# Optimization experiments

Hardware: AMD Instinct MI355X
Metric: run time of the kernel (lower is better)

The kernel has to match this reference:

```python
import jax, jax.numpy as jnp
import numpy as np

N_NODES = 100000
N_EDGES = 400000
IN_F, HID, OUT_F = 128, 1024, 64


def gcn_conv(x, src, dst, ew, W, b, n):
    # PyG GCNConv: add self-loops (weight 1), symmetric normalization,
    # out[dst] += norm * (x @ W)[src], then bias.
    loop = jnp.arange(n)
    s = jnp.concatenate([src, loop])
    d = jnp.concatenate([dst, loop])
    w = jnp.concatenate([ew, jnp.ones((n,), dtype=ew.dtype)])
    deg = jax.ops.segment_sum(w, d, num_segments=n)
    dinv = jnp.where(deg > 0, jax.lax.rsqrt(deg), 0.0)
    norm = dinv[s] * w * dinv[d]                      # [E+N]
    h = x @ W                                         # [N, out]
    out = jax.ops.segment_sum(h[s] * norm[:, None], d, num_segments=n)
    return out + b


def setup_inputs() -> dict:
    key = jax.random.key(0)
    k = jax.random.split(key, 8)
    x = jax.random.normal(k[0], (N_NODES, IN_F), dtype=jnp.float32)
    edge_index = jax.random.randint(k[1], (2, N_EDGES), 0, N_NODES, dtype=jnp.int64)
    edge_weight = jax.random.uniform(k[2], (N_EDGES,), dtype=jnp.float32)
    # Glorot-ish init for params
    W1 = jax.random.normal(k[3], (IN_F, HID), dtype=jnp.float32) * (1.0 / np.sqrt(IN_F))
    b1 = jnp.zeros((HID,), dtype=jnp.float32)
    W2 = jax.random.normal(k[4], (HID, OUT_F), dtype=jnp.float32) * (1.0 / np.sqrt(HID))
    b2 = jnp.zeros((OUT_F,), dtype=jnp.float32)
    return {"x": x, "edge_index": edge_index, "edge_weight": edge_weight,
            "W1": W1, "b1": b1, "W2": W2, "b2": b2}


def reference(x, edge_index, edge_weight, W1, b1, W2, b2):
    src, dst = edge_index[0], edge_index[1]
    h = gcn_conv(x, src, dst, edge_weight, W1, b1, N_NODES)
    h = jax.nn.relu(h)
    # F.dropout with training=False is identity (eval mode)
    out = gcn_conv(h, src, dst, edge_weight, W2, b2, N_NODES)
    return out
```

## Files before the change

### kernel.cpp

```cpp
#include <hip/hip_runtime.h>
#include <hip/hip_bf16.h>

#define N_NODES 100000
#define N_EDGES 400000
#define IN_F    128
#define HID     1024
#define OUT_F   64
#define BUCKET_CAP 24

typedef __attribute__((ext_vector_type(8))) short short8;
typedef __attribute__((ext_vector_type(4))) float floatx4;

__device__ inline unsigned short f2bf(float f) {
    unsigned int u = __float_as_uint(f);
    unsigned int r = u + 0x7FFF + ((u >> 16) & 1);
    return (unsigned short)(r >> 16);
}

__device__ inline float bf2f(unsigned int lo16) {
    return __uint_as_float(lo16 << 16);
}

__device__ __forceinline__ void gload_lds16(const void* g, void* l) {
    __builtin_amdgcn_global_load_lds(
        (const __attribute__((address_space(1))) void*)g,
        (__attribute__((address_space(3))) void*)l, 16, 0, 0);
}


__global__ void init_kernel(float* __restrict__ deg, int* __restrict__ cnt, int n) {
    int i = blockIdx.x * blockDim.x + threadIdx.x;
    if (i < n) { deg[i] = 1.0f; cnt[i] = 0; }
}

__global__ void deg_accum_kernel(const int* __restrict__ dst, const float* __restrict__ w,
                                 float* __restrict__ deg, int E) {
    int e = blockIdx.x * blockDim.x + threadIdx.x;
    if (e < E) atomicAdd(&deg[dst[e]], w[e]);
}

__global__ void rsqrt_inplace_kernel(float* __restrict__ deg, int n) {
    int i = blockIdx.x * blockDim.x + threadIdx.x;
    if (i < n) deg[i] = rsqrtf(deg[i]);
}

__global__ void fill_pairs_kernel(const int* __restrict__ src, const int* __restrict__ dst,
                                  const float* __restrict__ w, const float* __restrict__ dinv,
                                  int* __restrict__ cnt, int2* __restrict__ pairs, int E) {
    int e = blockIdx.x * blockDim.x + threadIdx.x;
    if (e < E) {
        int s = src[e];
        int d = dst[e];
        float nv = dinv[s] * w[e] * dinv[d];
        int slot = atomicAdd(&cnt[d], 1);
        if (slot < BUCKET_CAP)
            pairs[(long)d * BUCKET_CAP + slot] = make_int2(s, __float_as_int(nv));
    }
}


__global__ void convert_xb_kernel(const float* __restrict__ in, unsigned short* __restrict__ out, long n8) {
    long i = (long)blockIdx.x * blockDim.x + threadIdx.x;
    if (i < n8) {
        float4 a = ((const float4*)in)[i * 2];
        float4 b = ((const float4*)in)[i * 2 + 1];
        unsigned int q0 = (unsigned int)f2bf(a.x) | ((unsigned int)f2bf(a.y) << 16);
        unsigned int q1 = (unsigned int)f2bf(a.z) | ((unsigned int)f2bf(a.w) << 16);
        unsigned int q2 = (unsigned int)f2bf(b.x) | ((unsigned int)f2bf(b.y) << 16);
        unsigned int q3 = (unsigned int)f2bf(b.z) | ((unsigned int)f2bf(b.w) << 16);
        ((uint4*)out)[i] = make_uint4(q0, q1, q2, q3);
    }
}


__global__ __launch_bounds__(256) void gather128_kernel(
    const int2* __restrict__ pairs, const int* __restrict__ cnt,
    const float* __restrict__ dinv, const unsigned short* __restrict__ xb,
    unsigned short* __restrict__ xab)
{
    int node = blockIdx.x * 4 + (threadIdx.x >> 6);
    int l = threadIdx.x & 63;
    float di = dinv[node];
    float s = di * di;
    unsigned int uv = ((const unsigned int*)(xb + (long)node * IN_F))[l];
    float2 acc;
    acc.x = bf2f(uv & 0xffffu) * s;
    acc.y = bf2f(uv >> 16) * s;
    int c = cnt[node]; c = c < BUCKET_CAP ? c : BUCKET_CAP;
    const int2* p = pairs + (long)node * BUCKET_CAP;
    int j = 0;
    for (; j + 4 <= c; j += 4) {
        int2 p0 = p[j], p1 = p[j + 1], p2 = p[j + 2], p3 = p[j + 3];
        unsigned int u0 = ((const unsigned int*)(xb + (long)p0.x * IN_F))[l];
        unsigned int u1 = ((const unsigned int*)(xb + (long)p1.x * IN_F))[l];
        unsigned int u2 = ((const unsigned int*)(xb + (long)p2.x * IN_F))[l];
        unsigned int u3 = ((const unsigned int*)(xb + (long)p3.x * IN_F))[l];
        float n0 = __int_as_float(p0.y), n1 = __int_as_float(p1.y);
        float n2 = __int_as_float(p2.y), n3 = __int_as_float(p3.y);
        acc.x += n0 * bf2f(u0 & 0xffffu) + n1 * bf2f(u1 & 0xffffu)
               + n2 * bf2f(u2 & 0xffffu) + n3 * bf2f(u3 & 0xffffu);
        acc.y += n0 * bf2f(u0 >> 16) + n1 * bf2f(u1 >> 16)
               + n2 * bf2f(u2 >> 16) + n3 * bf2f(u3 >> 16);
    }
    for (; j < c; j++) {
        int2 pp = p[j];
        float nv = __int_as_float(pp.y);
        unsigned int u = ((const unsigned int*)(xb + (long)pp.x * IN_F))[l];
        acc.x += nv * bf2f(u & 0xffffu);
        acc.y += nv * bf2f(u >> 16);
    }
    unsigned int pk = (unsigned int)f2bf(acc.x) | ((unsigned int)f2bf(acc.y) << 16);
    ((unsigned int*)(xab + (long)node * IN_F))[l] = pk;
}

__global__ __launch_bounds__(256) void gather64_kernel(
    const int2* __restrict__ pairs, const int* __restrict__ cnt,
    const float* __restrict__ dinv, const unsigned short* __restrict__ tb,
    const float* __restrict__ bias, float* __restrict__ out)
{
    int node = blockIdx.x * 8 + (threadIdx.x >> 5);
    int l = threadIdx.x & 31;
    float di = dinv[node];
    float s = di * di;
    unsigned int tv = ((const unsigned int*)(tb + (long)node * OUT_F))[l];
    float2 bb = ((const float2*)bias)[l];
    float2 acc;
    acc.x = bf2f(tv & 0xffffu) * s + bb.x;
    acc.y = bf2f(tv >> 16) * s + bb.y;
    int c = cnt[node]; c = c < BUCKET_CAP ? c : BUCKET_CAP;
    const int2* p = pairs + (long)node * BUCKET_CAP;
    int j = 0;
    for (; j + 4 <= c; j += 4) {
        int2 p0 = p[j], p1 = p[j + 1], p2 = p[j + 2], p3 = p[j + 3];
        unsigned int u0 = ((const unsigned int*)(tb + (long)p0.x * OUT_F))[l];
        unsigned int u1 = ((const unsigned int*)(tb + (long)p1.x * OUT_F))[l];
        unsigned int u2 = ((const unsigned int*)(tb + (long)p2.x * OUT_F))[l];
        unsigned int u3 = ((const unsigned int*)(tb + (long)p3.x * OUT_F))[l];
        float n0 = __int_as_float(p0.y), n1 = __int_as_float(p1.y);
        float n2 = __int_as_float(p2.y), n3 = __int_as_float(p3.y);
        acc.x += n0 * bf2f(u0 & 0xffffu) + n1 * bf2f(u1 & 0xffffu)
               + n2 * bf2f(u2 & 0xffffu) + n3 * bf2f(u3 & 0xffffu);
        acc.y += n0 * bf2f(u0 >> 16) + n1 * bf2f(u1 >> 16)
               + n2 * bf2f(u2 >> 16) + n3 * bf2f(u3 >> 16);
    }
    for (; j < c; j++) {
        int2 pp = p[j];
        float nv = __int_as_float(pp.y);
        unsigned int u = ((const unsigned int*)(tb + (long)pp.x * OUT_F))[l];
        acc.x += nv * bf2f(u & 0xffffu);
        acc.y += nv * bf2f(u >> 16);
    }
    ((float2*)(out + (long)node * OUT_F))[l] = acc;
}


__global__ void convert_wstream_kernel(const float* __restrict__ W1, const float* __restrict__ W2,
                                       unsigned short* __restrict__ S) {
    int r = blockIdx.x * blockDim.x + threadIdx.x;
    int c = blockIdx.y;
    int f = r >> 9;
    int l = (r >> 3) & 63;
    int j = r & 7;
    float v;
    if (f < 16) {
        int nt = f >> 2, kt = f & 3;
        int hid = c * 64 + nt * 16 + (l & 15);
        int k   = kt * 32 + (l >> 4) * 8 + j;
        v = W1[(long)k * HID + hid];
    } else {
        int f2 = f - 16;
        int kb = f2 >> 2, nt = f2 & 3;
        int kh = c * 64 + kb * 32 + (l >> 4) * 8 + j;
        int oc = nt * 16 + (l & 15);
        v = W2[(long)kh * OUT_F + oc];
    }
    S[(long)c * 12288 + r] = f2bf(v);
}


__global__ __launch_bounds__(512, 2) void fused_mlp_mfma_kernel(
    const unsigned short* __restrict__ Xb, const unsigned short* __restrict__ Wstream,
    const float* __restrict__ b1, unsigned short* __restrict__ Tb, int M)
{
    __shared__ unsigned short Wbuf[2][12288];
    __shared__ unsigned short Hs[8][4096];

    const int tid = threadIdx.x;
    const int w   = tid >> 6;
    const int l   = tid & 63;
    const int lr  = l & 15;
    const int lq  = l >> 4;
    const int swz = (lr & 7) << 4;
    const long row0 = (long)blockIdx.x * 512 + w * 64;

    short8 bx[4][4];
    #pragma unroll
    for (int rt = 0; rt < 4; rt++) {
        long row = row0 + rt * 16 + lr;
        if (row < M) {
            const unsigned short* p = Xb + row * IN_F + lq * 8;
            #pragma unroll
            for (int kt = 0; kt < 4; kt++)
                bx[rt][kt] = *(const short8*)(p + kt * 32);
        } else {
            #pragma unroll
            for (int kt = 0; kt < 4; kt++)
                #pragma unroll
                for (int j = 0; j < 8; j++) bx[rt][kt][j] = 0;
        }
    }

    {
        const unsigned short* g = Wstream + (long)(w * 3) * 512 + l * 8;
        unsigned short* d = &Wbuf[0][(w * 3) * 512];
        #pragma unroll
        for (int s = 0; s < 3; s++)
            gload_lds16(g + s * 512, d + s * 512);
    }
    __syncthreads();

    floatx4 tacc[4][4];
    #pragma unroll
    for (int rt = 0; rt < 4; rt++)
        #pragma unroll
        for (int nt = 0; nt < 4; nt++)
            tacc[rt][nt] = (floatx4)0.0f;

    for (int c = 0; c < 16; c++) {
        const int cur = c & 1;

        if (c < 15) {
            const unsigned short* g = Wstream + (long)(c + 1) * 12288 + (long)(w * 3) * 512 + l * 8;
            unsigned short* d = &Wbuf[cur ^ 1][(w * 3) * 512];
            #pragma unroll
            for (int s = 0; s < 3; s++)
                gload_lds16(g + s * 512, d + s * 512);
        }

        const unsigned short* Wb = &Wbuf[cur][0];
        char* slab = (char*)&Hs[w][0];

        #pragma unroll
        for (int nt = 0; nt < 4; nt++) {
            short8 w1f[4];
            #pragma unroll
            for (int kt = 0; kt < 4; kt++)
                w1f[kt] = *(const short8*)(Wb + (nt * 4 + kt) * 512 + l * 8);

            floatx4 hacc[4];
            #pragma unroll
            for (int rt = 0; rt < 4; rt++) hacc[rt] = (floatx4)0.0f;

            #pragma unroll
            for (int kt = 0; kt < 4; kt++)
                #pragma unroll
                for (int rt = 0; rt < 4; rt++)
                    hacc[rt] = __builtin_amdgcn_mfma_f32_16x16x32_bf16(w1f[kt], bx[rt][kt], hacc[rt], 0, 0, 0);

            floatx4 bb = *(const floatx4*)(b1 + c * 64 + nt * 16 + lq * 4);
            #pragma unroll
            for (int rt = 0; rt < 4; rt++) {
                float h0 = fmaxf(hacc[rt][0] + bb[0], 0.0f);
                float h1 = fmaxf(hacc[rt][1] + bb[1], 0.0f);
                float h2 = fmaxf(hacc[rt][2] + bb[2], 0.0f);
                float h3 = fmaxf(hacc[rt][3] + bb[3], 0.0f);
                unsigned int p0 = (unsigned int)f2bf(h0) | ((unsigned int)f2bf(h1) << 16);
                unsigned int p1 = (unsigned int)f2bf(h2) | ((unsigned int)f2bf(h3) << 16);
                int off = (rt * 16 + lr) * 128 + (((nt * 32) + lq * 8) ^ swz);
                *(uint2*)(slab + off) = make_uint2(p0, p1);
            }
        }

        short8 hf[4][2];
        #pragma unroll
        for (int rt = 0; rt < 4; rt++)
            #pragma unroll
            for (int kb = 0; kb < 2; kb++) {
                int off = (rt * 16 + lr) * 128 + ((kb * 64 + lq * 16) ^ swz);
                hf[rt][kb] = *(const short8*)(slab + off);
            }

        #pragma unroll
        for (int kb = 0; kb < 2; kb++) {
            #pragma unroll
            for (int nt = 0; nt < 4; nt++) {
                short8 w2f = *(const short8*)(Wb + (16 + kb * 4 + nt) * 512 + l * 8);
                #pragma unroll
                for (int rt = 0; rt < 4; rt++)
                    tacc[rt][nt] = __builtin_amdgcn_mfma_f32_16x16x32_bf16(w2f, hf[rt][kb], tacc[rt][nt], 0, 0, 0);
            }
        }

        if (c < 15) __syncthreads();
    }

    #pragma unroll
    for (int rt = 0; rt < 4; rt++) {
        long row = row0 + rt * 16 + lr;
        if (row < M) {
            #pragma unroll
            for (int nt = 0; nt < 4; nt++) {
                unsigned int q0 = (unsigned int)f2bf(tacc[rt][nt][0]) | ((unsigned int)f2bf(tacc[rt][nt][1]) << 16);
                unsigned int q1 = (unsigned int)f2bf(tacc[rt][nt][2]) | ((unsigned int)f2bf(tacc[rt][nt][3]) << 16);
                *(uint2*)(Tb + row * OUT_F + nt * 16 + lq * 4) = make_uint2(q0, q1);
            }
        }
    }
}


extern "C" void kernel_launch(void* const* d_in, const int* in_sizes, int n_in,
                              void* d_out, int out_size, void* d_ws, size_t ws_size,
                              hipStream_t stream) {
    const float* x   = (const float*)d_in[0];
    const int*   src = (const int*)d_in[1];
    const int*   dst = ((const int*)d_in[1]) + N_EDGES;
    const float* ew  = (const float*)d_in[2];
    const float* W1  = (const float*)d_in[3];
    const float* b1  = (const float*)d_in[4];
    const float* W2  = (const float*)d_in[5];
    const float* b2  = (const float*)d_in[6];
    float* out = (float*)d_out;

    float* ws     = (float*)d_ws;
    float* dinv   = ws;
    int*   cnt    = (int*)(ws + 100096);
    int2*  pairs  = (int2*)(ws + 200192);
    unsigned short* xb  = (unsigned short*)(ws + 5000192);
    unsigned short* xab = (unsigned short*)(ws + 11400192);
    unsigned short* tb  = (unsigned short*)(ws + 17800192);
    unsigned short* wstream = (unsigned short*)(ws + 21000192);

    const int B = 256;

    init_kernel<<<(N_NODES + B - 1) / B, B, 0, stream>>>(dinv, cnt, N_NODES);
    deg_accum_kernel<<<(N_EDGES + B - 1) / B, B, 0, stream>>>(dst, ew, dinv, N_EDGES);
    convert_xb_kernel<<<(int)(((long)N_NODES * IN_F / 8 + B - 1) / B), B, 0, stream>>>(
        x, xb, (long)N_NODES * IN_F / 8);
    convert_wstream_kernel<<<dim3(48, 16), B, 0, stream>>>(W1, W2, wstream);
    rsqrt_inplace_kernel<<<(N_NODES + B - 1) / B, B, 0, stream>>>(dinv, N_NODES);
    fill_pairs_kernel<<<(N_EDGES + B - 1) / B, B, 0, stream>>>(src, dst, ew, dinv, cnt, pairs, N_EDGES);

    gather128_kernel<<<N_NODES / 4, 256, 0, stream>>>(pairs, cnt, dinv, xb, xab);

    fused_mlp_mfma_kernel<<<(N_NODES + 511) / 512, 512, 0, stream>>>(
        xab, wstream, b1, tb, N_NODES);

    gather64_kernel<<<N_NODES / 8, 256, 0, stream>>>(pairs, cnt, dinv, tb, b2, out);
}
```

Before: 188.7 us.

## Halve rows per block and single-buffer weights to raise MLP kernel occupancy

The fused MLP kernel now processes 256 rows per block (32 per wave) instead of 512, drops the double-buffered weight LDS tile to a single buffer, and halves the per-wave hidden slab. Launch bounds change from 2 to 4 blocks per CU, so more waves can be resident and register and LDS pressure drop. In exchange the weight stream is re-read by twice as many blocks, and without double buffering each chunk's global-to-LDS load is exposed behind an extra barrier rather than overlapped with compute.

```diff
diff --git a/kernel.cpp b/kernel.cpp
--- a/kernel.cpp
+++ b/kernel.cpp
@@ -178,12 +178,12 @@
 }
 
 
-__global__ __launch_bounds__(512, 2) void fused_mlp_mfma_kernel(
+__global__ __launch_bounds__(512, 4) void fused_mlp_mfma_kernel(
     const unsigned short* __restrict__ Xb, const unsigned short* __restrict__ Wstream,
     const float* __restrict__ b1, unsigned short* __restrict__ Tb, int M)
 {
-    __shared__ unsigned short Wbuf[2][12288];
-    __shared__ unsigned short Hs[8][4096];
+    __shared__ unsigned short Wbuf[12288];
+    __shared__ unsigned short Hs[8][2048];
 
     const int tid = threadIdx.x;
     const int w   = tid >> 6;
@@ -191,11 +191,11 @@
     const int lr  = l & 15;
     const int lq  = l >> 4;
     const int swz = (lr & 7) << 4;
-    const long row0 = (long)blockIdx.x * 512 + w * 64;
-
-    short8 bx[4][4];
+    const long row0 = (long)blockIdx.x * 256 + w * 32;
+
+    short8 bx[2][4];
     #pragma unroll
-    for (int rt = 0; rt < 4; rt++) {
+    for (int rt = 0; rt < 2; rt++) {
         long row = row0 + rt * 16 + lr;
         if (row < M) {
             const unsigned short* p = Xb + row * IN_F + lq * 8;
@@ -212,33 +212,31 @@
 
     {
         const unsigned short* g = Wstream + (long)(w * 3) * 512 + l * 8;
-        unsigned short* d = &Wbuf[0][(w * 3) * 512];
+        unsigned short* d = &Wbuf[(w * 3) * 512];
         #pragma unroll
         for (int s = 0; s < 3; s++)
             gload_lds16(g + s * 512, d + s * 512);
     }
-    __syncthreads();
-
-    floatx4 tacc[4][4];
+
+    floatx4 tacc[2][4];
     #pragma unroll
-    for (int rt = 0; rt < 4; rt++)
+    for (int rt = 0; rt < 2; rt++)
         #pragma unroll
         for (int nt = 0; nt < 4; nt++)
             tacc[rt][nt] = (floatx4)0.0f;
 
     for (int c = 0; c < 16; c++) {
-        const int cur = c & 1;
-
-        if (c < 15) {
-            const unsigned short* g = Wstream + (long)(c + 1) * 12288 + (long)(w * 3) * 512 + l * 8;
-            unsigned short* d = &Wbuf[cur ^ 1][(w * 3) * 512];
-            #pragma unroll
-            for (int s = 0; s < 3; s++)
-                gload_lds16(g + s * 512, d + s * 512);
-        }
-
-        const unsigned short* Wb = &Wbuf[cur][0];
+        __syncthreads();
+
+        const unsigned short* Wb = &Wbuf[0];
         char* slab = (char*)&Hs[w][0];
+
+        floatx4 hacc[2][4];
+        #pragma unroll
+        for (int rt = 0; rt < 2; rt++)
+            #pragma unroll
+            for (int nt = 0; nt < 4; nt++)
+                hacc[rt][nt] = (floatx4)0.0f;
 
         #pragma unroll
         for (int nt = 0; nt < 4; nt++) {
@@ -246,24 +244,22 @@
             #pragma unroll
             for (int kt = 0; kt < 4; kt++)
                 w1f[kt] = *(const short8*)(Wb + (nt * 4 + kt) * 512 + l * 8);
-
-            floatx4 hacc[4];
-            #pragma unroll
-            for (int rt = 0; rt < 4; rt++) hacc[rt] = (floatx4)0.0f;
-
-            #pragma unroll
-            for (int kt = 0; kt < 4; kt++)
-                #pragma unroll
-                for (int rt = 0; rt < 4; rt++)
-                    hacc[rt] = __builtin_amdgcn_mfma_f32_16x16x32_bf16(w1f[kt], bx[rt][kt], hacc[rt], 0, 0, 0);
-
+            #pragma unroll
+            for (int kt = 0; kt < 4; kt++) {
+                hacc[0][nt] = __builtin_amdgcn_mfma_f32_16x16x32_bf16(w1f[kt], bx[0][kt], hacc[0][nt], 0, 0, 0);
+                hacc[1][nt] = __builtin_amdgcn_mfma_f32_16x16x32_bf16(w1f[kt], bx[1][kt], hacc[1][nt], 0, 0, 0);
+            }
+        }
+
+        #pragma unroll
+        for (int nt = 0; nt < 4; nt++) {
             floatx4 bb = *(const floatx4*)(b1 + c * 64 + nt * 16 + lq * 4);
             #pragma unroll
-            for (int rt = 0; rt < 4; rt++) {
-                float h0 = fmaxf(hacc[rt][0] + bb[0], 0.0f);
-                float h1 = fmaxf(hacc[rt][1] + bb[1], 0.0f);
-                float h2 = fmaxf(hacc[rt][2] + bb[2], 0.0f);
-                float h3 = fmaxf(hacc[rt][3] + bb[3], 0.0f);
+            for (int rt = 0; rt < 2; rt++) {
+                float h0 = fmaxf(hacc[rt][nt][0] + bb[0], 0.0f);
+                float h1 = fmaxf(hacc[rt][nt][1] + bb[1], 0.0f);
+                float h2 = fmaxf(hacc[rt][nt][2] + bb[2], 0.0f);
+                float h3 = fmaxf(hacc[rt][nt][3] + bb[3], 0.0f);
                 unsigned int p0 = (unsigned int)f2bf(h0) | ((unsigned int)f2bf(h1) << 16);
                 unsigned int p1 = (unsigned int)f2bf(h2) | ((unsigned int)f2bf(h3) << 16);
                 int off = (rt * 16 + lr) * 128 + (((nt * 32) + lq * 8) ^ swz);
@@ -271,9 +267,9 @@
             }
         }
 
-        short8 hf[4][2];
-        #pragma unroll
-        for (int rt = 0; rt < 4; rt++)
+        short8 hf[2][2];
+        #pragma unroll
+        for (int rt = 0; rt < 2; rt++)
             #pragma unroll
             for (int kb = 0; kb < 2; kb++) {
                 int off = (rt * 16 + lr) * 128 + ((kb * 64 + lq * 16) ^ swz);
@@ -285,17 +281,23 @@
             #pragma unroll
             for (int nt = 0; nt < 4; nt++) {
                 short8 w2f = *(const short8*)(Wb + (16 + kb * 4 + nt) * 512 + l * 8);
-                #pragma unroll
-                for (int rt = 0; rt < 4; rt++)
-                    tacc[rt][nt] = __builtin_amdgcn_mfma_f32_16x16x32_bf16(w2f, hf[rt][kb], tacc[rt][nt], 0, 0, 0);
-            }
-        }
-
-        if (c < 15) __syncthreads();
+                tacc[0][nt] = __builtin_amdgcn_mfma_f32_16x16x32_bf16(w2f, hf[0][kb], tacc[0][nt], 0, 0, 0);
+                tacc[1][nt] = __builtin_amdgcn_mfma_f32_16x16x32_bf16(w2f, hf[1][kb], tacc[1][nt], 0, 0, 0);
+            }
+        }
+
+        if (c < 15) {
+            __syncthreads();
+            const unsigned short* g = Wstream + (long)(c + 1) * 12288 + (long)(w * 3) * 512 + l * 8;
+            unsigned short* d = &Wbuf[(w * 3) * 512];
+            #pragma unroll
+            for (int s = 0; s < 3; s++)
+                gload_lds16(g + s * 512, d + s * 512);
+        }
     }
 
     #pragma unroll
-    for (int rt = 0; rt < 4; rt++) {
+    for (int rt = 0; rt < 2; rt++) {
         long row = row0 + rt * 16 + lr;
         if (row < M) {
             #pragma unroll
@@ -343,7 +345,7 @@
 
     gather128_kernel<<<N_NODES / 4, 256, 0, stream>>>(pairs, cnt, dinv, xb, xab);
 
-    fused_mlp_mfma_kernel<<<(N_NODES + 511) / 512, 512, 0, stream>>>(
+    fused_mlp_mfma_kernel<<<(N_NODES + 255) / 256, 512, 0, stream>>>(
         xab, wstream, b1, tb, N_NODES);
 
     gather64_kernel<<<N_NODES / 8, 256, 0, stream>>>(pairs, cnt, dinv, tb, b2, out);
```

After: 184.6 us. 1.02x faster.
